# Performance work log

Hardware: AMD Instinct MI355X
Metric: run time of the kernel (lower is better)

The kernel has to match this reference:

```python
import jax, jax.numpy as jnp
import numpy as np

N = 50000   # num_nodes
E = 250000  # edges per view
D = 128     # in_dim = h_dim = out_dim
B = 4       # num_bases
RELS = (8, 12, 6)


def setup_inputs() -> dict:
    key = jax.random.key(0)
    ks = iter(jax.random.split(key, 64))
    s = 1.0 / np.sqrt(D)
    inp = {"node_features": jax.random.normal(next(ks), (N, D), jnp.float32) * 0.1}
    for v, R in enumerate(RELS, start=1):
        inp[f"src{v}"] = jax.random.randint(next(ks), (E,), 0, N)
        inp[f"dst{v}"] = jax.random.randint(next(ks), (E,), 0, N)
        inp[f"rel{v}"] = jax.random.randint(next(ks), (E,), 0, R)
        for l in (1, 2):
            inp[f"v{v}_bases{l}"] = jax.random.normal(next(ks), (B, D, D), jnp.float32) * s
            inp[f"v{v}_coef{l}"] = jax.random.normal(next(ks), (R, B), jnp.float32) * 0.5
            inp[f"v{v}_loopw{l}"] = jax.random.normal(next(ks), (D, D), jnp.float32) * s
            inp[f"v{v}_bias{l}"] = jnp.zeros((D,), jnp.float32)
    inp["fusion_w"] = jax.random.normal(next(ks), (3 * D, D), jnp.float32) * (1.0 / np.sqrt(3 * D))
    inp["fusion_b"] = jnp.zeros((D,), jnp.float32)
    return inp


def rgcn_layer(h, src, dst, rel, bases, coef, loop_w, bias, act):
    # basis trick: project nodes through all bases once, then combine per edge
    node_proj = jnp.einsum('ni,bio->nbo', h, bases)          # [N,B,out]
    msg = jnp.einsum('eb,ebo->eo', coef[rel], node_proj[src])  # [E,out]
    agg = jax.ops.segment_sum(msg, dst, num_segments=h.shape[0])
    out = agg + h @ loop_w + bias                             # self-loop + bias (DGL defaults)
    return jax.nn.relu(out) if act else out


def single_view(feats, src, dst, rel, bases1, coef1, loopw1, bias1,
                bases2, coef2, loopw2, bias2):
    h = rgcn_layer(feats, src, dst, rel, bases1, coef1, loopw1, bias1, act=True)
    return rgcn_layer(h, src, dst, rel, bases2, coef2, loopw2, bias2, act=False)


def reference(node_features,
              src1, dst1, rel1, src2, dst2, rel2, src3, dst3, rel3,
              v1_bases1, v1_coef1, v1_loopw1, v1_bias1,
              v1_bases2, v1_coef2, v1_loopw2, v1_bias2,
              v2_bases1, v2_coef1, v2_loopw1, v2_bias1,
              v2_bases2, v2_coef2, v2_loopw2, v2_bias2,
              v3_bases1, v3_coef1, v3_loopw1, v3_bias1,
              v3_bases2, v3_coef2, v3_loopw2, v3_bias2,
              fusion_w, fusion_b):
    h1 = single_view(node_features, src1, dst1, rel1,
                     v1_bases1, v1_coef1, v1_loopw1, v1_bias1,
                     v1_bases2, v1_coef2, v1_loopw2, v1_bias2)
    h2 = single_view(node_features, src2, dst2, rel2,
                     v2_bases1, v2_coef1, v2_loopw1, v2_bias1,
                     v2_bases2, v2_coef2, v2_loopw2, v2_bias2)
    h3 = single_view(node_features, src3, dst3, rel3,
                     v3_bases1, v3_coef1, v3_loopw1, v3_bias1,
                     v3_bases2, v3_coef2, v3_loopw2, v3_bias2)
    h_cat = jnp.concatenate([h1, h2, h3], axis=-1)  # [N, 3*D]
    return h_cat @ fusion_w + fusion_b
```

## Files before the change

kernel.cpp:

```cpp
#include <hip/hip_runtime.h>
#include <hip/hip_bf16.h>
#include <stdint.h>

typedef _Float16 f16x8 __attribute__((ext_vector_type(8)));
typedef _Float16 f16x2 __attribute__((ext_vector_type(2)));
typedef float f32x4 __attribute__((ext_vector_type(4)));

#define AL 136

struct PrepDesc { const float* src; _Float16* dst; int dstride; };
struct PrepArgs { PrepDesc d[33]; };

__global__ __launch_bounds__(256) void prep_weights(PrepArgs args) {
    __shared__ _Float16 lds[128 * 129];
    const PrepDesc de = args.d[blockIdx.x];
    int t = threadIdx.x;
    for (int q = 0; q < 64; ++q) {
        int li = t + q * 256;
        int i = li >> 7, o = li & 127;
        lds[o * 129 + i] = (_Float16)de.src[li];
    }
    __syncthreads();
    for (int q = 0; q < 64; ++q) {
        int lo = t + q * 256;
        int o = lo >> 7, i = lo & 127;
        de.dst[(size_t)o * de.dstride + i] = lds[o * 129 + i];
    }
}

__global__ __launch_bounds__(256) void f32_to_f16(const float* __restrict__ in,
                                                  _Float16* __restrict__ out, int n4) {
    int i = blockIdx.x * 256 + threadIdx.x;
    if (i >= n4) return;
    float4 v = *((const float4*)in + i);
    f16x2 a, b;
    a[0] = (_Float16)v.x; a[1] = (_Float16)v.y;
    b[0] = (_Float16)v.z; b[1] = (_Float16)v.w;
    f16x2* o = (f16x2*)out + i * 2;
    o[0] = a; o[1] = b;
}

struct EdgeArgs {
    const int* src[3]; const int* dst[3]; const int* rel[3];
    int E[3]; int N;
};

__global__ __launch_bounds__(256) void zero_deg(int* __restrict__ deg3, int n) {
    int i = blockIdx.x * 256 + threadIdx.x;
    if (i < n) deg3[i] = 0;
}

__global__ __launch_bounds__(256) void hist3(EdgeArgs ea, int* __restrict__ deg3) {
    int v = blockIdx.y;
    const int* dst = ea.dst[v];
    int* deg = deg3 + (size_t)v * ea.N;
    for (int e = blockIdx.x * 256 + threadIdx.x; e < ea.E[v]; e += gridDim.x * 256)
        atomicAdd(&deg[dst[e]], 1);
}

__global__ __launch_bounds__(256) void scan1_kernel(const int* __restrict__ deg,
                                                    int* __restrict__ off,
                                                    int* __restrict__ bsum, int n) {
    __shared__ int s[256];
    int b = blockIdx.x, t = threadIdx.x;
    int base = b * 2048 + t * 8;
    int v[8]; int sum = 0;
    for (int j = 0; j < 8; ++j) {
        int x = (base + j < n) ? deg[base + j] : 0;
        v[j] = sum;
        sum += x;
    }
    s[t] = sum;
    __syncthreads();
    for (int st = 1; st < 256; st <<= 1) {
        int y = (t >= st) ? s[t - st] : 0;
        __syncthreads();
        s[t] += y;
        __syncthreads();
    }
    int texcl = t ? s[t - 1] : 0;
    if (t == 255) bsum[b] = s[255];
    for (int j = 0; j < 8; ++j)
        if (base + j < n) off[base + j] = texcl + v[j];
}

__global__ __launch_bounds__(256) void scan2_kernel(int* __restrict__ off,
                                                    int* __restrict__ cur,
                                                    const int* __restrict__ bsum,
                                                    int n, int Etot) {
    __shared__ int pref;
    int b = blockIdx.x, t = threadIdx.x;
    if (t == 0) { int p = 0; for (int j = 0; j < b; ++j) p += bsum[j]; pref = p; }
    __syncthreads();
    int p = pref;
    int base = b * 2048 + t * 8;
    for (int j = 0; j < 8; ++j)
        if (base + j < n) { int x = off[base + j] + p; off[base + j] = x; cur[base + j] = x; }
    if (b == 0 && t == 0) off[n] = Etot;
}

__global__ __launch_bounds__(256) void scatter3(EdgeArgs ea, int* __restrict__ cur3,
                                                int* __restrict__ packed3) {
    int v = blockIdx.y;
    const int* src = ea.src[v];
    const int* dst = ea.dst[v];
    const int* rel = ea.rel[v];
    int* cur = cur3 + (size_t)v * ea.N;
    for (int e = blockIdx.x * 256 + threadIdx.x; e < ea.E[v]; e += gridDim.x * 256) {
        int pos = atomicAdd(&cur[dst[e]], 1);
        packed3[pos] = src[e] | (rel[e] << 20);
    }
}

struct GatherArgs {
    const int* off3;
    const int* packed3;
    const float* coef[3];
    const _Float16* h[3];
    _Float16* T;
    int N; size_t Tvs;
};

__global__ __launch_bounds__(256) void gather3(GatherArgs g) {
    int v = blockIdx.y;
    int node = (blockIdx.x << 2) | (threadIdx.x >> 6);
    if (node >= g.N) return;
    int lane = threadIdx.x & 63;
    const int* off = g.off3 + (size_t)v * g.N;
    const float* coef = g.coef[v];
    const _Float16* h = g.h[v];
    _Float16* T = g.T + (size_t)v * g.Tvs;

    int i  = __builtin_amdgcn_readfirstlane(off[node]);
    int e1 = __builtin_amdgcn_readfirstlane(off[node + 1]);
    float acc[8] = {};

    for (; i + 3 < e1; i += 4) {
        int p0 = __builtin_amdgcn_readfirstlane(g.packed3[i]);
        int p1 = __builtin_amdgcn_readfirstlane(g.packed3[i + 1]);
        int p2 = __builtin_amdgcn_readfirstlane(g.packed3[i + 2]);
        int p3 = __builtin_amdgcn_readfirstlane(g.packed3[i + 3]);
        int s0 = p0 & 0xFFFFF, r0 = p0 >> 20;
        int s1 = p1 & 0xFFFFF, r1 = p1 >> 20;
        int s2 = p2 & 0xFFFFF, r2 = p2 >> 20;
        int s3 = p3 & 0xFFFFF, r3 = p3 >> 20;
        uint32_t q0 = ((const uint32_t*)(h + (size_t)s0 * 128))[lane];
        uint32_t q1 = ((const uint32_t*)(h + (size_t)s1 * 128))[lane];
        uint32_t q2 = ((const uint32_t*)(h + (size_t)s2 * 128))[lane];
        uint32_t q3 = ((const uint32_t*)(h + (size_t)s3 * 128))[lane];
        float4 c0 = *(const float4*)(coef + (size_t)r0 * 4);
        float4 c1 = *(const float4*)(coef + (size_t)r1 * 4);
        float4 c2 = *(const float4*)(coef + (size_t)r2 * 4);
        float4 c3 = *(const float4*)(coef + (size_t)r3 * 4);
        f16x2 u0 = __builtin_bit_cast(f16x2, q0);
        f16x2 u1 = __builtin_bit_cast(f16x2, q1);
        f16x2 u2 = __builtin_bit_cast(f16x2, q2);
        f16x2 u3 = __builtin_bit_cast(f16x2, q3);
        float lo0 = (float)u0[0], hi0 = (float)u0[1];
        float lo1 = (float)u1[0], hi1 = (float)u1[1];
        float lo2 = (float)u2[0], hi2 = (float)u2[1];
        float lo3 = (float)u3[0], hi3 = (float)u3[1];
        acc[0] += c0.x * lo0 + c1.x * lo1 + c2.x * lo2 + c3.x * lo3;
        acc[1] += c0.x * hi0 + c1.x * hi1 + c2.x * hi2 + c3.x * hi3;
        acc[2] += c0.y * lo0 + c1.y * lo1 + c2.y * lo2 + c3.y * lo3;
        acc[3] += c0.y * hi0 + c1.y * hi1 + c2.y * hi2 + c3.y * hi3;
        acc[4] += c0.z * lo0 + c1.z * lo1 + c2.z * lo2 + c3.z * lo3;
        acc[5] += c0.z * hi0 + c1.z * hi1 + c2.z * hi2 + c3.z * hi3;
        acc[6] += c0.w * lo0 + c1.w * lo1 + c2.w * lo2 + c3.w * lo3;
        acc[7] += c0.w * hi0 + c1.w * hi1 + c2.w * hi2 + c3.w * hi3;
    }
    for (; i < e1; ++i) {
        int p0 = __builtin_amdgcn_readfirstlane(g.packed3[i]);
        int s0 = p0 & 0xFFFFF, r0 = p0 >> 20;
        uint32_t q0 = ((const uint32_t*)(h + (size_t)s0 * 128))[lane];
        float4 c0 = *(const float4*)(coef + (size_t)r0 * 4);
        f16x2 u0 = __builtin_bit_cast(f16x2, q0);
        float lo0 = (float)u0[0], hi0 = (float)u0[1];
        acc[0] += c0.x * lo0;  acc[1] += c0.x * hi0;
        acc[2] += c0.y * lo0;  acc[3] += c0.y * hi0;
        acc[4] += c0.z * lo0;  acc[5] += c0.z * hi0;
        acc[6] += c0.w * lo0;  acc[7] += c0.w * hi0;
    }
    _Float16* tb = T + (size_t)node * 512 + 2 * lane;
    for (int b = 0; b < 4; ++b) {
        f16x2 o; o[0] = (_Float16)acc[2 * b]; o[1] = (_Float16)acc[2 * b + 1];
        *(f16x2*)(tb + b * 128) = o;
    }
}

struct GemmArgs {
    const _Float16* T;
    const _Float16* hin[3];
    const _Float16* WT[3];
    const float* bias[3];
    _Float16* hout;
    int M; int relu; size_t Tvs; size_t hovs;
};

__global__ __launch_bounds__(512) void gemm_layer(GemmArgs ga) {
    __shared__ _Float16 As[64 * AL];
    __shared__ _Float16 Bs[128 * AL];
    int v = blockIdx.y;
    const _Float16* Tb  = ga.T + (size_t)v * ga.Tvs;
    const _Float16* hin = ga.hin[v];
    const _Float16* BT  = ga.WT[v];
    const float* bias   = ga.bias[v];
    _Float16* out       = ga.hout + (size_t)v * ga.hovs;
    int M = ga.M;

    int tid = threadIdx.x;
    int m0 = blockIdx.x * 64;
    int wid = tid >> 6, lane = tid & 63;
    int wr = (wid >> 2) * 32;
    int wc = (wid & 3) * 32;
    int lm = lane & 15;
    int lk = (lane >> 4) * 8;

    f32x4 acc[2][2] = {};

    for (int kb = 0; kb < 5; ++kb) {
        const _Float16* Asrc; size_t astride;
        if (kb < 4) { Asrc = Tb + (size_t)kb * 128; astride = 512; }
        else        { Asrc = hin;                   astride = 128; }
        for (int q = 0; q < 2; ++q) {
            int li = tid + q * 512;
            int r = li >> 4;
            int c = (li & 15) << 3;
            int gr = m0 + r; if (gr >= M) gr = M - 1;
            *(f16x8*)(As + r * AL + c) = *(const f16x8*)(Asrc + (size_t)gr * astride + c);
        }
        for (int q = 0; q < 4; ++q) {
            int li = tid + q * 512;
            int r = li >> 4;
            int c = (li & 15) << 3;
            *(f16x8*)(Bs + r * AL + c) = *(const f16x8*)(BT + (size_t)r * 640 + kb * 128 + c);
        }
        __syncthreads();

        for (int ks = 0; ks < 4; ++ks) {
            f16x8 a[2], b[2];
            for (int mi = 0; mi < 2; ++mi)
                a[mi] = *(const f16x8*)(As + (wr + mi * 16 + lm) * AL + ks * 32 + lk);
            for (int ni = 0; ni < 2; ++ni)
                b[ni] = *(const f16x8*)(Bs + (wc + ni * 16 + lm) * AL + ks * 32 + lk);
            for (int mi = 0; mi < 2; ++mi)
                for (int ni = 0; ni < 2; ++ni)
                    acc[mi][ni] = __builtin_amdgcn_mfma_f32_16x16x32_f16(a[mi], b[ni], acc[mi][ni], 0, 0, 0);
        }
        __syncthreads();
    }

    int rbase = (lane >> 4) * 4;
    for (int mi = 0; mi < 2; ++mi) {
        for (int j = 0; j < 4; ++j) {
            int gr = m0 + wr + mi * 16 + rbase + j;
            if (gr >= M) continue;
            for (int ni = 0; ni < 2; ++ni) {
                int col = wc + ni * 16 + lm;
                float val = acc[mi][ni][j] + bias[col];
                if (ga.relu) val = fmaxf(val, 0.f);
                out[(size_t)gr * 128 + col] = (_Float16)val;
            }
        }
    }
}

struct FusArgs {
    const _Float16* A[3];
    const _Float16* BT;
    const float* bias;
    float* out; int M;
};

__global__ __launch_bounds__(256) void gemm_fusion(FusArgs fa) {
    __shared__ _Float16 As[128 * AL];
    __shared__ _Float16 Bs[128 * AL];
    int tid = threadIdx.x;
    int m0 = blockIdx.x * 128;
    int M = fa.M;
    int wid = tid >> 6, lane = tid & 63;
    int wr = (wid >> 1) * 64;
    int wc = (wid & 1) * 64;
    int lm = lane & 15;
    int lk = (lane >> 4) * 8;

    f32x4 acc[4][4] = {};

    for (int kb = 0; kb < 3; ++kb) {
        const _Float16* Asrc = fa.A[kb];
        for (int q = 0; q < 8; ++q) {
            int li = tid + q * 256;
            int r = li >> 4;
            int c = (li & 15) << 3;
            int gr = m0 + r; if (gr >= M) gr = M - 1;
            *(f16x8*)(As + r * AL + c) = *(const f16x8*)(Asrc + (size_t)gr * 128 + c);
        }
        for (int q = 0; q < 8; ++q) {
            int li = tid + q * 256;
            int r = li >> 4;
            int c = (li & 15) << 3;
            *(f16x8*)(Bs + r * AL + c) = *(const f16x8*)(fa.BT + (size_t)r * 384 + kb * 128 + c);
        }
        __syncthreads();

        for (int ks = 0; ks < 4; ++ks) {
            f16x8 a[4], b[4];
            for (int mi = 0; mi < 4; ++mi)
                a[mi] = *(const f16x8*)(As + (wr + mi * 16 + lm) * AL + ks * 32 + lk);
            for (int ni = 0; ni < 4; ++ni)
                b[ni] = *(const f16x8*)(Bs + (wc + ni * 16 + lm) * AL + ks * 32 + lk);
            for (int mi = 0; mi < 4; ++mi)
                for (int ni = 0; ni < 4; ++ni)
                    acc[mi][ni] = __builtin_amdgcn_mfma_f32_16x16x32_f16(a[mi], b[ni], acc[mi][ni], 0, 0, 0);
        }
        __syncthreads();
    }

    int rbase = (lane >> 4) * 4;
    for (int mi = 0; mi < 4; ++mi) {
        for (int j = 0; j < 4; ++j) {
            int gr = m0 + wr + mi * 16 + rbase + j;
            if (gr >= M) continue;
            for (int ni = 0; ni < 4; ++ni) {
                int col = wc + ni * 16 + lm;
                fa.out[(size_t)gr * 128 + col] = acc[mi][ni][j] + fa.bias[col];
            }
        }
    }
}

extern "C" void kernel_launch(void* const* d_in, const int* in_sizes, int n_in,
                              void* d_out, int out_size, void* d_ws, size_t ws_size,
                              hipStream_t stream) {
    const int D = 128;
    const int M = in_sizes[0] / D;

    struct ViewIn {
        const int *src, *dst, *rel;
        const float *bases1, *coef1, *loopw1, *bias1;
        const float *bases2, *coef2, *loopw2, *bias2;
        int E;
    } V[3];
    int idx = 1;
    for (int v = 0; v < 3; ++v) {
        V[v].src    = (const int*)d_in[idx + 0];
        V[v].dst    = (const int*)d_in[idx + 1];
        V[v].rel    = (const int*)d_in[idx + 2];
        V[v].bases1 = (const float*)d_in[idx + 3];
        V[v].coef1  = (const float*)d_in[idx + 4];
        V[v].loopw1 = (const float*)d_in[idx + 5];
        V[v].bias1  = (const float*)d_in[idx + 6];
        V[v].bases2 = (const float*)d_in[idx + 7];
        V[v].coef2  = (const float*)d_in[idx + 8];
        V[v].loopw2 = (const float*)d_in[idx + 9];
        V[v].bias2  = (const float*)d_in[idx + 10];
        V[v].E      = in_sizes[idx + 0];
        idx += 11;
    }
    const float* fusion_w = (const float*)d_in[idx];
    const float* fusion_b = (const float*)d_in[idx + 1];
    int Etot = V[0].E + V[1].E + V[2].E;

    char* w = (char*)d_ws;
    auto alloc = [&](size_t bytes) -> char* {
        char* p = w; w += (bytes + 255) & ~(size_t)255; return p;
    };
    _Float16* nf16 = (_Float16*)alloc((size_t)M * 128 * 2);
    _Float16* wts  = (_Float16*)alloc((size_t)(6 * 81920 + 49152) * 2);
    int* deg3      = (int*)alloc((size_t)3 * M * 4);
    int* cur3      = (int*)alloc((size_t)3 * M * 4);
    int* bsum      = (int*)alloc(512);
    int* off3      = (int*)alloc(((size_t)3 * M + 1) * 4);
    int* packed3   = (int*)alloc((size_t)Etot * 4);
    _Float16* T3   = (_Float16*)alloc((size_t)3 * M * 512 * 2);
    _Float16* h1b  = (_Float16*)alloc((size_t)3 * M * 128 * 2);
    _Float16* h2b  = (_Float16*)alloc((size_t)3 * M * 128 * 2);

    _Float16 *WT[3][2];
    for (int v = 0; v < 3; ++v)
        for (int l = 0; l < 2; ++l)
            WT[v][l] = wts + (size_t)(v * 2 + l) * 81920;
    _Float16* fusTcat = wts + 6 * 81920;

    PrepArgs pa;
    int t = 0;
    for (int v = 0; v < 3; ++v) {
        const float* bases[2] = { V[v].bases1, V[v].bases2 };
        const float* loopw[2] = { V[v].loopw1, V[v].loopw2 };
        for (int l = 0; l < 2; ++l) {
            for (int b = 0; b < 4; ++b) {
                pa.d[t].src = bases[l] + (size_t)b * 16384;
                pa.d[t].dst = WT[v][l] + (size_t)b * 128;
                pa.d[t].dstride = 640; ++t;
            }
            pa.d[t].src = loopw[l];
            pa.d[t].dst = WT[v][l] + 512;
            pa.d[t].dstride = 640; ++t;
        }
    }
    for (int v = 0; v < 3; ++v) {
        pa.d[t].src = fusion_w + (size_t)v * 16384;
        pa.d[t].dst = fusTcat + (size_t)v * 128;
        pa.d[t].dstride = 384; ++t;
    }
    prep_weights<<<33, 256, 0, stream>>>(pa);

    int n4 = M * D / 4;
    f32_to_f16<<<(n4 + 255) / 256, 256, 0, stream>>>((const float*)d_in[0], nf16, n4);

    EdgeArgs ea;
    for (int v = 0; v < 3; ++v) {
        ea.src[v] = V[v].src; ea.dst[v] = V[v].dst; ea.rel[v] = V[v].rel; ea.E[v] = V[v].E;
    }
    ea.N = M;
    int n3 = 3 * M;
    zero_deg<<<(n3 + 255) / 256, 256, 0, stream>>>(deg3, n3);
    hist3<<<dim3(512, 3), 256, 0, stream>>>(ea, deg3);
    int nsb = (n3 + 2047) / 2048;
    scan1_kernel<<<nsb, 256, 0, stream>>>(deg3, off3, bsum, n3);
    scan2_kernel<<<nsb, 256, 0, stream>>>(off3, cur3, bsum, n3, Etot);
    scatter3<<<dim3(512, 3), 256, 0, stream>>>(ea, cur3, packed3);

    int ng  = (M + 3) / 4;
    int gxL = (M + 63) / 64;
    int gxF = (M + 127) / 128;
    size_t Tvs = (size_t)M * 512;
    size_t hvs = (size_t)M * 128;
    float* outF = (float*)d_out;

    GatherArgs g1;
    g1.off3 = off3; g1.packed3 = packed3; g1.T = T3; g1.N = M; g1.Tvs = Tvs;
    for (int v = 0; v < 3; ++v) { g1.coef[v] = V[v].coef1; g1.h[v] = nf16; }
    gather3<<<dim3(ng, 3), 256, 0, stream>>>(g1);

    GemmArgs m1;
    m1.T = T3; m1.hout = h1b; m1.M = M; m1.relu = 1; m1.Tvs = Tvs; m1.hovs = hvs;
    for (int v = 0; v < 3; ++v) { m1.hin[v] = nf16; m1.WT[v] = WT[v][0]; m1.bias[v] = V[v].bias1; }
    gemm_layer<<<dim3(gxL, 3), 512, 0, stream>>>(m1);

    GatherArgs g2 = g1;
    for (int v = 0; v < 3; ++v) { g2.coef[v] = V[v].coef2; g2.h[v] = h1b + (size_t)v * hvs; }
    gather3<<<dim3(ng, 3), 256, 0, stream>>>(g2);

    GemmArgs m2;
    m2.T = T3; m2.hout = h2b; m2.M = M; m2.relu = 0; m2.Tvs = Tvs; m2.hovs = hvs;
    for (int v = 0; v < 3; ++v) { m2.hin[v] = h1b + (size_t)v * hvs; m2.WT[v] = WT[v][1]; m2.bias[v] = V[v].bias2; }
    gemm_layer<<<dim3(gxL, 3), 512, 0, stream>>>(m2);

    FusArgs fa;
    for (int v = 0; v < 3; ++v) fa.A[v] = h2b + (size_t)v * hvs;
    fa.BT = fusTcat; fa.bias = fusion_b; fa.out = outF; fa.M = M;
    gemm_fusion<<<gxF, 256, 0, stream>>>(fa);
}
```

Before: 335.5 us.

## Pre-swizzle f16 activations and weights in global memory; stage GEMM tiles via global_load_lds

```diff
diff --git a/kernel.cpp b/kernel.cpp
--- a/kernel.cpp
+++ b/kernel.cpp
@@ -6,7 +6,12 @@
 typedef _Float16 f16x2 __attribute__((ext_vector_type(2)));
 typedef float f32x4 __attribute__((ext_vector_type(4)));
 
-#define AL 136
+
+__device__ __forceinline__ void gll16(const _Float16* g, _Float16* l) {
+    __builtin_amdgcn_global_load_lds(
+        (const __attribute__((address_space(1))) void*)g,
+        (__attribute__((address_space(3))) void*)l, 16, 0, 0);
+}
 
 struct PrepDesc { const float* src; _Float16* dst; int dstride; };
 struct PrepArgs { PrepDesc d[33]; };
@@ -24,7 +29,7 @@
     for (int q = 0; q < 64; ++q) {
         int lo = t + q * 256;
         int o = lo >> 7, i = lo & 127;
-        de.dst[(size_t)o * de.dstride + i] = lds[o * 129 + i];
+        de.dst[(size_t)o * de.dstride + (i ^ ((o & 7) << 3))] = lds[o * 129 + i];
     }
 }
 
@@ -33,11 +38,15 @@
     int i = blockIdx.x * 256 + threadIdx.x;
     if (i >= n4) return;
     float4 v = *((const float4*)in + i);
+    int n = i >> 5;
+    int c = (i & 31) * 4;
+    int cs = c ^ ((n & 7) << 3);
     f16x2 a, b;
     a[0] = (_Float16)v.x; a[1] = (_Float16)v.y;
     b[0] = (_Float16)v.z; b[1] = (_Float16)v.w;
-    f16x2* o = (f16x2*)out + i * 2;
-    o[0] = a; o[1] = b;
+    _Float16* o = out + (size_t)n * 128 + cs;
+    *(f16x2*)o = a;
+    *(f16x2*)(o + 2) = b;
 }
 
 struct EdgeArgs {
@@ -144,10 +153,10 @@
         int s1 = p1 & 0xFFFFF, r1 = p1 >> 20;
         int s2 = p2 & 0xFFFFF, r2 = p2 >> 20;
         int s3 = p3 & 0xFFFFF, r3 = p3 >> 20;
-        uint32_t q0 = ((const uint32_t*)(h + (size_t)s0 * 128))[lane];
-        uint32_t q1 = ((const uint32_t*)(h + (size_t)s1 * 128))[lane];
-        uint32_t q2 = ((const uint32_t*)(h + (size_t)s2 * 128))[lane];
-        uint32_t q3 = ((const uint32_t*)(h + (size_t)s3 * 128))[lane];
+        uint32_t q0 = ((const uint32_t*)(h + (size_t)s0 * 128))[lane ^ ((s0 & 7) << 2)];
+        uint32_t q1 = ((const uint32_t*)(h + (size_t)s1 * 128))[lane ^ ((s1 & 7) << 2)];
+        uint32_t q2 = ((const uint32_t*)(h + (size_t)s2 * 128))[lane ^ ((s2 & 7) << 2)];
+        uint32_t q3 = ((const uint32_t*)(h + (size_t)s3 * 128))[lane ^ ((s3 & 7) << 2)];
         float4 c0 = *(const float4*)(coef + (size_t)r0 * 4);
         float4 c1 = *(const float4*)(coef + (size_t)r1 * 4);
         float4 c2 = *(const float4*)(coef + (size_t)r2 * 4);
@@ -172,7 +181,7 @@
     for (; i < e1; ++i) {
         int p0 = __builtin_amdgcn_readfirstlane(g.packed3[i]);
         int s0 = p0 & 0xFFFFF, r0 = p0 >> 20;
-        uint32_t q0 = ((const uint32_t*)(h + (size_t)s0 * 128))[lane];
+        uint32_t q0 = ((const uint32_t*)(h + (size_t)s0 * 128))[lane ^ ((s0 & 7) << 2)];
         float4 c0 = *(const float4*)(coef + (size_t)r0 * 4);
         f16x2 u0 = __builtin_bit_cast(f16x2, q0);
         float lo0 = (float)u0[0], hi0 = (float)u0[1];
@@ -181,7 +190,8 @@
         acc[4] += c0.z * lo0;  acc[5] += c0.z * hi0;
         acc[6] += c0.w * lo0;  acc[7] += c0.w * hi0;
     }
-    _Float16* tb = T + (size_t)node * 512 + 2 * lane;
+    int cs = (2 * lane) ^ ((node & 7) << 3);
+    _Float16* tb = T + (size_t)node * 512 + cs;
     for (int b = 0; b < 4; ++b) {
         f16x2 o; o[0] = (_Float16)acc[2 * b]; o[1] = (_Float16)acc[2 * b + 1];
         *(f16x2*)(tb + b * 128) = o;
@@ -198,8 +208,8 @@
 };
 
 __global__ __launch_bounds__(512) void gemm_layer(GemmArgs ga) {
-    __shared__ _Float16 As[64 * AL];
-    __shared__ _Float16 Bs[128 * AL];
+    __shared__ _Float16 As[64 * 128];
+    __shared__ _Float16 Bs[128 * 128];
     int v = blockIdx.y;
     const _Float16* Tb  = ga.T + (size_t)v * ga.Tvs;
     const _Float16* hin = ga.hin[v];
@@ -215,6 +225,7 @@
     int wc = (wid & 3) * 32;
     int lm = lane & 15;
     int lk = (lane >> 4) * 8;
+    int xm = (lm & 7) << 3;
 
     f32x4 acc[2][2] = {};
 
@@ -227,22 +238,22 @@
             int r = li >> 4;
             int c = (li & 15) << 3;
             int gr = m0 + r; if (gr >= M) gr = M - 1;
-            *(f16x8*)(As + r * AL + c) = *(const f16x8*)(Asrc + (size_t)gr * astride + c);
+            gll16(Asrc + (size_t)gr * astride + c, As + (size_t)li * 8);
         }
         for (int q = 0; q < 4; ++q) {
             int li = tid + q * 512;
-            int r = li >> 4;
-            int c = (li & 15) << 3;
-            *(f16x8*)(Bs + r * AL + c) = *(const f16x8*)(BT + (size_t)r * 640 + kb * 128 + c);
+            gll16(BT + (size_t)(li >> 4) * 640 + kb * 128 + ((li & 15) << 3),
+                  Bs + (size_t)li * 8);
         }
         __syncthreads();
 
         for (int ks = 0; ks < 4; ++ks) {
+            int ac = (ks * 32 + lk) ^ xm;
             f16x8 a[2], b[2];
             for (int mi = 0; mi < 2; ++mi)
-                a[mi] = *(const f16x8*)(As + (wr + mi * 16 + lm) * AL + ks * 32 + lk);
+                a[mi] = *(const f16x8*)(As + (wr + mi * 16 + lm) * 128 + ac);
             for (int ni = 0; ni < 2; ++ni)
-                b[ni] = *(const f16x8*)(Bs + (wc + ni * 16 + lm) * AL + ks * 32 + lk);
+                b[ni] = *(const f16x8*)(Bs + (wc + ni * 16 + lm) * 128 + ac);
             for (int mi = 0; mi < 2; ++mi)
                 for (int ni = 0; ni < 2; ++ni)
                     acc[mi][ni] = __builtin_amdgcn_mfma_f32_16x16x32_f16(a[mi], b[ni], acc[mi][ni], 0, 0, 0);
@@ -255,11 +266,12 @@
         for (int j = 0; j < 4; ++j) {
             int gr = m0 + wr + mi * 16 + rbase + j;
             if (gr >= M) continue;
+            int rs = (gr & 7) << 3;
             for (int ni = 0; ni < 2; ++ni) {
                 int col = wc + ni * 16 + lm;
                 float val = acc[mi][ni][j] + bias[col];
                 if (ga.relu) val = fmaxf(val, 0.f);
-                out[(size_t)gr * 128 + col] = (_Float16)val;
+                out[(size_t)gr * 128 + (col ^ rs)] = (_Float16)val;
             }
         }
     }
@@ -273,8 +285,8 @@
 };
 
 __global__ __launch_bounds__(256) void gemm_fusion(FusArgs fa) {
-    __shared__ _Float16 As[128 * AL];
-    __shared__ _Float16 Bs[128 * AL];
+    __shared__ _Float16 As[128 * 128];
+    __shared__ _Float16 Bs[128 * 128];
     int tid = threadIdx.x;
     int m0 = blockIdx.x * 128;
     int M = fa.M;
@@ -283,6 +295,7 @@
     int wc = (wid & 1) * 64;
     int lm = lane & 15;
     int lk = (lane >> 4) * 8;
+    int xm = (lm & 7) << 3;
 
     f32x4 acc[4][4] = {};
 
@@ -293,22 +306,22 @@
             int r = li >> 4;
             int c = (li & 15) << 3;
             int gr = m0 + r; if (gr >= M) gr = M - 1;
-            *(f16x8*)(As + r * AL + c) = *(const f16x8*)(Asrc + (size_t)gr * 128 + c);
+            gll16(Asrc + (size_t)gr * 128 + c, As + (size_t)li * 8);
         }
         for (int q = 0; q < 8; ++q) {
             int li = tid + q * 256;
-            int r = li >> 4;
-            int c = (li & 15) << 3;
-            *(f16x8*)(Bs + r * AL + c) = *(const f16x8*)(fa.BT + (size_t)r * 384 + kb * 128 + c);
+            gll16(fa.BT + (size_t)(li >> 4) * 384 + kb * 128 + ((li & 15) << 3),
+                  Bs + (size_t)li * 8);
         }
         __syncthreads();
 
         for (int ks = 0; ks < 4; ++ks) {
+            int ac = (ks * 32 + lk) ^ xm;
             f16x8 a[4], b[4];
             for (int mi = 0; mi < 4; ++mi)
-                a[mi] = *(const f16x8*)(As + (wr + mi * 16 + lm) * AL + ks * 32 + lk);
+                a[mi] = *(const f16x8*)(As + (wr + mi * 16 + lm) * 128 + ac);
             for (int ni = 0; ni < 4; ++ni)
-                b[ni] = *(const f16x8*)(Bs + (wc + ni * 16 + lm) * AL + ks * 32 + lk);
+                b[ni] = *(const f16x8*)(Bs + (wc + ni * 16 + lm) * 128 + ac);
             for (int mi = 0; mi < 4; ++mi)
                 for (int ni = 0; ni < 4; ++ni)
                     acc[mi][ni] = __builtin_amdgcn_mfma_f32_16x16x32_f16(a[mi], b[ni], acc[mi][ni], 0, 0, 0);
```

Result: no change. 331.7 us (-1.1%).
